# Kernel optimization log

Hardware: AMD Instinct MI355X
Metric: run time of the kernel (lower is better)

Reference implementation:

```python
import jax, jax.numpy as jnp
import numpy as np

D = 4096      # input_size == hidden_size (required by the broadcast add in the update)
T = 8192      # sequence length
F = 10        # num_factor (hard-coded in the module)
OUT = 10      # output_size
BETA = 0.1    # exponential scale for decay factors


def setup_inputs() -> dict:
    key = jax.random.key(0)
    ks = jax.random.split(key, 4)
    inp = jax.random.normal(ks[0], (T, 1, D), dtype=jnp.float32)
    hidden = jnp.zeros((1, F, D), dtype=jnp.float32)
    # decay factors: 1 - clip(Exp(beta), 0, 1-eps), each broadcast across hidden dim
    rng = np.random.default_rng(0)
    d = 1.0 - np.clip(rng.exponential(BETA, F), 0.0, 1.0 - np.finfo(np.float32).eps)
    w = jnp.broadcast_to(jnp.asarray(d, jnp.float32)[None, :, None], (1, F, D))
    pool_w = jax.random.normal(ks[1], (1, F, 1), jnp.float32) * (1.0 / np.sqrt(F))
    pool_b = jnp.zeros((1,), jnp.float32)
    H1 = (D + D) // 2  # (input_size + hidden_size) // 2
    i2o_w = jax.random.normal(ks[2], (H1, 2 * D), jnp.float32) * (1.0 / np.sqrt(2 * D))
    i2o_b = jnp.zeros((H1,), jnp.float32)
    o_w = jax.random.normal(ks[3], (OUT, H1), jnp.float32) * (1.0 / np.sqrt(H1))
    o_b = jnp.zeros((OUT,), jnp.float32)
    return dict(inp=inp, hidden=hidden, w=w, pool_w=pool_w, pool_b=pool_b,
                i2o_w=i2o_w, i2o_b=i2o_b, o_w=o_w, o_b=o_b)


def reference(inp, hidden, w, pool_w, pool_b, i2o_w, i2o_b, o_w, o_b):
    # inp: [T, 1, D]; hidden: [1, F, D] decay-state
    Tn = inp.shape[0]

    def step(carry, xt):
        h, hsum = carry
        hsum = hsum + h                   # pre-update hidden feeds the pooled feature
        h_new = w * h + xt[:, None, :]    # decay-weighted update, x broadcast over factors
        return (h_new, hsum), None

    (h_final, h_sum), _ = jax.lax.scan(step, (hidden, jnp.zeros_like(hidden)), inp)

    # Conv1d(F, 1, 1) pooling is linear -> sum over time of pool(h_t) = pool(sum_t h_t)
    pooled_sum = jnp.einsum('f,bfd->bd', pool_w[0, :, 0], h_sum) + Tn * pool_b  # [1, D]
    x_sum = inp.sum(axis=0)  # [1, D]

    # avg_feature at the last step = cumulative sum of combined / steps
    avg = jnp.concatenate([x_sum, pooled_sum], axis=1) / Tn  # [1, 2D]
    pred = jax.nn.relu(avg @ i2o_w.T + i2o_b) @ o_w.T + o_b  # [1, OUT]
    return pred, h_final
```

## Files before the change

kernel.cpp:

```cpp
#include <hip/hip_runtime.h>

#define TLEN 8192
#define DD   4096
#define NF   10
#define NC   12
#define NACC 12

__device__ __forceinline__ double powi_d(double w, int n) {
    double a = 1.0, p = w;
    while (n) { if (n & 1) a *= p; p *= p; n >>= 1; }
    return a;
}

__global__ void coef_kernel(const float* __restrict__ w,
                            const float* __restrict__ pool_w,
                            float* __restrict__ coef) {
    int t = blockIdx.x * blockDim.x + threadIdx.x;
    if (t >= TLEN) return;
    int n = TLEN - 1 - t;
    double g = 0.0;
#pragma unroll
    for (int f = 0; f < NF; ++f) {
        double wf = (double)w[(size_t)f * DD];
        double a  = powi_d(wf, n);
        double den = 1.0 - wf;
        double c  = (den > 1e-30) ? (1.0 - a) / den : (double)n;
        g += (double)pool_w[f] * c;
        coef[t * NC + f] = (float)a;
    }
    coef[t * NC + NF]     = (float)g;
    coef[t * NC + NF + 1] = 0.0f;
}

__global__ __launch_bounds__(256) void pass_kernel(const float* __restrict__ inp,
                                                   const float* __restrict__ coef,
                                                   float* __restrict__ part,
                                                   int rows) {
    __shared__ float sc[256 * NC];
    const int t0 = blockIdx.y * rows;
    const int d  = blockIdx.x * 1024 + threadIdx.x * 4;

    float sx=0,sy=0,sz=0,sw=0;
    float px=0,py=0,pz=0,pw4=0;
    float hx[NF], hy[NF], hz[NF], hw[NF];
#pragma unroll
    for (int f = 0; f < NF; ++f) { hx[f]=0; hy[f]=0; hz[f]=0; hw[f]=0; }

    const float* ip = inp + (size_t)t0 * DD + d;

    for (int rbase = 0; rbase < rows; rbase += 256) {
        int rcnt = rows - rbase; if (rcnt > 256) rcnt = 256;
        __syncthreads();
        for (int i = threadIdx.x; i < rcnt * NC; i += 256)
            sc[i] = coef[(size_t)(t0 + rbase) * NC + i];
        __syncthreads();
        for (int r = 0; r < rcnt; ++r) {
            float4 x = *(const float4*)ip;
            ip += DD;
            const float* cf = &sc[r * NC];
            sx += x.x; sy += x.y; sz += x.z; sw += x.w;
            float g = cf[NF];
            px  = fmaf(g, x.x, px);  py  = fmaf(g, x.y, py);
            pz  = fmaf(g, x.z, pz);  pw4 = fmaf(g, x.w, pw4);
#pragma unroll
            for (int f = 0; f < NF; ++f) {
                float a = cf[f];
                hx[f] = fmaf(a, x.x, hx[f]); hy[f] = fmaf(a, x.y, hy[f]);
                hz[f] = fmaf(a, x.z, hz[f]); hw[f] = fmaf(a, x.w, hw[f]);
            }
        }
    }

    size_t base = ((size_t)blockIdx.y * NC) * DD + d;
    *(float4*)(part + base)      = make_float4(sx, sy, sz, sw);
    *(float4*)(part + base + DD) = make_float4(px, py, pz, pw4);
#pragma unroll
    for (int f = 0; f < NF; ++f)
        *(float4*)(part + base + (size_t)(2 + f) * DD) =
            make_float4(hx[f], hy[f], hz[f], hw[f]);
}

__global__ void reduce_kernel(const float* __restrict__ part,
                              float* __restrict__ red, int C) {
    int idx = blockIdx.x * blockDim.x + threadIdx.x;
    if (idx >= NACC * DD) return;
    float s = 0.0f;
    for (int c = 0; c < C; ++c)
        s += part[(size_t)c * NC * DD + idx];
    red[idx] = s;
}

__global__ void finalize_kernel(const float* __restrict__ red,
                                const float* __restrict__ w,
                                const float* __restrict__ pool_w,
                                const float* __restrict__ pool_b,
                                const float* __restrict__ hidden,
                                float* __restrict__ out,
                                float* __restrict__ avg) {
    int i = blockIdx.x * blockDim.x + threadIdx.x;
    int d = i * 4;
    float4 xs = *(const float4*)(red + d);
    float4 pl = *(const float4*)(red + DD + d);
    const float invT = 1.0f / (float)TLEN;
#pragma unroll
    for (int f = 0; f < NF; ++f) {
        double wf = (double)w[(size_t)f * DD];
        double wTd = powi_d(wf, TLEN);
        double den = 1.0 - wf;
        double sTd = (den > 1e-30) ? (1.0 - wTd) / den : (double)TLEN;
        float wT = (float)wTd;
        float pwsT = (float)((double)pool_w[f] * sTd);
        float4 hf = *(const float4*)(red + (size_t)(2 + f) * DD + d);
        float4 h0 = *(const float4*)(hidden + (size_t)f * DD + d);
        hf.x = fmaf(wT, h0.x, hf.x); hf.y = fmaf(wT, h0.y, hf.y);
        hf.z = fmaf(wT, h0.z, hf.z); hf.w = fmaf(wT, h0.w, hf.w);
        pl.x = fmaf(pwsT, h0.x, pl.x); pl.y = fmaf(pwsT, h0.y, pl.y);
        pl.z = fmaf(pwsT, h0.z, pl.z); pl.w = fmaf(pwsT, h0.w, pl.w);
        float* o = out + 10 + (size_t)f * DD + d;
        o[0] = hf.x; o[1] = hf.y; o[2] = hf.z; o[3] = hf.w;
    }
    float pb = pool_b[0];
    avg[d+0] = xs.x * invT; avg[d+1] = xs.y * invT;
    avg[d+2] = xs.z * invT; avg[d+3] = xs.w * invT;
    avg[DD + d + 0] = pl.x * invT + pb; avg[DD + d + 1] = pl.y * invT + pb;
    avg[DD + d + 2] = pl.z * invT + pb; avg[DD + d + 3] = pl.w * invT + pb;
}

__global__ __launch_bounds__(256) void gemv_kernel(const float* __restrict__ W,
                                                   const float* __restrict__ b,
                                                   const float* __restrict__ avg,
                                                   float* __restrict__ hid) {
    int row  = blockIdx.x * 4 + (threadIdx.x >> 6);
    int lane = threadIdx.x & 63;
    const float* wr = W + (size_t)row * (2 * DD);
    float acc = 0.0f;
#pragma unroll 8
    for (int j0 = 0; j0 < 32; ++j0) {
        int j = j0 * 256 + lane * 4;
        float4 wv = *(const float4*)(wr + j);
        float4 av = *(const float4*)(avg + j);
        acc = fmaf(wv.x, av.x, acc); acc = fmaf(wv.y, av.y, acc);
        acc = fmaf(wv.z, av.z, acc); acc = fmaf(wv.w, av.w, acc);
    }
    for (int off = 32; off; off >>= 1) acc += __shfl_down(acc, off, 64);
    if (lane == 0) hid[row] = fmaxf(acc + b[row], 0.0f);
}

__global__ void out_kernel(const float* __restrict__ hid,
                           const float* __restrict__ ow,
                           const float* __restrict__ ob,
                           float* __restrict__ out) {
    __shared__ float redl[256];
    int o = blockIdx.x;
    float acc = 0.0f;
    for (int h = threadIdx.x; h < DD; h += 256)
        acc = fmaf(hid[h], ow[(size_t)o * DD + h], acc);
    redl[threadIdx.x] = acc;
    __syncthreads();
    for (int s = 128; s; s >>= 1) {
        if (threadIdx.x < s) redl[threadIdx.x] += redl[threadIdx.x + s];
        __syncthreads();
    }
    if (threadIdx.x == 0) out[o] = redl[0] + ob[o];
}

extern "C" void kernel_launch(void* const* d_in, const int* in_sizes, int n_in,
                              void* d_out, int out_size, void* d_ws, size_t ws_size,
                              hipStream_t stream) {
    const float* inp    = (const float*)d_in[0];
    const float* hidden = (const float*)d_in[1];
    const float* w      = (const float*)d_in[2];
    const float* pw     = (const float*)d_in[3];
    const float* pb     = (const float*)d_in[4];
    const float* i2o_w  = (const float*)d_in[5];
    const float* i2o_b  = (const float*)d_in[6];
    const float* o_w    = (const float*)d_in[7];
    const float* o_b    = (const float*)d_in[8];
    float* out = (float*)d_out;
    float* ws  = (float*)d_ws;

    float* coef = ws;
    float* red  = ws + 98304;
    float* avg  = ws + 147456;
    float* hid  = ws + 155648;
    float* part = ws + 159744;

    int C = 128;
    while (C > 1) {
        size_t need = (159744 + (size_t)C * NC * DD) * sizeof(float);
        if (need <= ws_size) break;
        C >>= 1;
    }
    int rows = TLEN / C;

    coef_kernel<<<TLEN / 256, 256, 0, stream>>>(w, pw, coef);
    pass_kernel<<<dim3(4, C), 256, 0, stream>>>(inp, coef, part, rows);
    reduce_kernel<<<(NACC * DD + 255) / 256, 256, 0, stream>>>(part, red, C);
    finalize_kernel<<<4, 256, 0, stream>>>(red, w, pw, pb, hidden, out, avg);
    gemv_kernel<<<DD / 4, 256, 0, stream>>>(i2o_w, i2o_b, avg, hid);
    out_kernel<<<10, 256, 0, stream>>>(hid, o_w, o_b, out);
}
```

Baseline: 113.4 us.

## Fuse coefficient computation into pass kernel, prefetch rows, stage avg in LDS

```diff
diff --git a/kernel.cpp b/kernel.cpp
--- a/kernel.cpp
+++ b/kernel.cpp
@@ -12,33 +12,35 @@
     return a;
 }
 
-__global__ void coef_kernel(const float* __restrict__ w,
-                            const float* __restrict__ pool_w,
-                            float* __restrict__ coef) {
-    int t = blockIdx.x * blockDim.x + threadIdx.x;
-    if (t >= TLEN) return;
-    int n = TLEN - 1 - t;
-    double g = 0.0;
-#pragma unroll
-    for (int f = 0; f < NF; ++f) {
-        double wf = (double)w[(size_t)f * DD];
-        double a  = powi_d(wf, n);
-        double den = 1.0 - wf;
-        double c  = (den > 1e-30) ? (1.0 - a) / den : (double)n;
-        g += (double)pool_w[f] * c;
-        coef[t * NC + f] = (float)a;
-    }
-    coef[t * NC + NF]     = (float)g;
-    coef[t * NC + NF + 1] = 0.0f;
-}
-
 __global__ __launch_bounds__(256) void pass_kernel(const float* __restrict__ inp,
-                                                   const float* __restrict__ coef,
+                                                   const float* __restrict__ w,
+                                                   const float* __restrict__ pool_w,
                                                    float* __restrict__ part,
                                                    int rows) {
     __shared__ float sc[256 * NC];
+    __shared__ float scg[256 * NF];
     const int t0 = blockIdx.y * rows;
-    const int d  = blockIdx.x * 1024 + threadIdx.x * 4;
+
+    for (int i = threadIdx.x; i < rows * NF; i += 256) {
+        int r = i / NF, f = i - r * NF;
+        double wf = (double)w[(size_t)f * DD];
+        int n = TLEN - 1 - (t0 + r);
+        double a = powi_d(wf, n);
+        double den = 1.0 - wf;
+        sc[r * NC + f] = (float)a;
+        scg[i] = (float)((den > 1e-12) ? (double)pool_w[f] * (1.0 - a) / den
+                                       : (double)pool_w[f] * (double)n);
+    }
+    __syncthreads();
+    if (threadIdx.x < rows) {
+        float g = 0.0f;
+#pragma unroll
+        for (int f = 0; f < NF; ++f) g += scg[threadIdx.x * NF + f];
+        sc[threadIdx.x * NC + NF] = g;
+    }
+    __syncthreads();
+
+    const int d = blockIdx.x * 1024 + threadIdx.x * 4;
 
     float sx=0,sy=0,sz=0,sw=0;
     float px=0,py=0,pz=0,pw4=0;
@@ -46,30 +48,37 @@
 #pragma unroll
     for (int f = 0; f < NF; ++f) { hx[f]=0; hy[f]=0; hz[f]=0; hw[f]=0; }
 
+    auto PROC = [&](int r, float4 x) {
+        const float* cf = &sc[r * NC];
+        sx += x.x; sy += x.y; sz += x.z; sw += x.w;
+        float g = cf[NF];
+        px  = fmaf(g, x.x, px);  py  = fmaf(g, x.y, py);
+        pz  = fmaf(g, x.z, pz);  pw4 = fmaf(g, x.w, pw4);
+#pragma unroll
+        for (int f = 0; f < NF; ++f) {
+            float a = cf[f];
+            hx[f] = fmaf(a, x.x, hx[f]); hy[f] = fmaf(a, x.y, hy[f]);
+            hz[f] = fmaf(a, x.z, hz[f]); hw[f] = fmaf(a, x.w, hw[f]);
+        }
+    };
+
     const float* ip = inp + (size_t)t0 * DD + d;
-
-    for (int rbase = 0; rbase < rows; rbase += 256) {
-        int rcnt = rows - rbase; if (rcnt > 256) rcnt = 256;
-        __syncthreads();
-        for (int i = threadIdx.x; i < rcnt * NC; i += 256)
-            sc[i] = coef[(size_t)(t0 + rbase) * NC + i];
-        __syncthreads();
-        for (int r = 0; r < rcnt; ++r) {
-            float4 x = *(const float4*)ip;
-            ip += DD;
-            const float* cf = &sc[r * NC];
-            sx += x.x; sy += x.y; sz += x.z; sw += x.w;
-            float g = cf[NF];
-            px  = fmaf(g, x.x, px);  py  = fmaf(g, x.y, py);
-            pz  = fmaf(g, x.z, pz);  pw4 = fmaf(g, x.w, pw4);
-#pragma unroll
-            for (int f = 0; f < NF; ++f) {
-                float a = cf[f];
-                hx[f] = fmaf(a, x.x, hx[f]); hy[f] = fmaf(a, x.y, hy[f]);
-                hz[f] = fmaf(a, x.z, hz[f]); hw[f] = fmaf(a, x.w, hw[f]);
-            }
-        }
-    }
+    float4 xa = *(const float4*)(ip);
+    float4 xb = *(const float4*)(ip + DD);
+    float4 xc = *(const float4*)(ip + 2 * DD);
+    float4 xd = *(const float4*)(ip + 3 * DD);
+    ip += 4 * (size_t)DD;
+    int r = 0;
+    for (; r + 4 < rows; r += 4) {
+        float4 ya = *(const float4*)(ip);
+        float4 yb = *(const float4*)(ip + DD);
+        float4 yc = *(const float4*)(ip + 2 * DD);
+        float4 yd = *(const float4*)(ip + 3 * DD);
+        ip += 4 * (size_t)DD;
+        PROC(r + 0, xa); PROC(r + 1, xb); PROC(r + 2, xc); PROC(r + 3, xd);
+        xa = ya; xb = yb; xc = yc; xd = yd;
+    }
+    PROC(r + 0, xa); PROC(r + 1, xb); PROC(r + 2, xc); PROC(r + 3, xd);
 
     size_t base = ((size_t)blockIdx.y * NC) * DD + d;
     *(float4*)(part + base)      = make_float4(sx, sy, sz, sw);
@@ -107,7 +116,7 @@
         double wf = (double)w[(size_t)f * DD];
         double wTd = powi_d(wf, TLEN);
         double den = 1.0 - wf;
-        double sTd = (den > 1e-30) ? (1.0 - wTd) / den : (double)TLEN;
+        double sTd = (den > 1e-12) ? (1.0 - wTd) / den : (double)TLEN;
         float wT = (float)wTd;
         float pwsT = (float)((double)pool_w[f] * sTd);
         float4 hf = *(const float4*)(red + (size_t)(2 + f) * DD + d);
@@ -130,18 +139,27 @@
                                                    const float* __restrict__ b,
                                                    const float* __restrict__ avg,
                                                    float* __restrict__ hid) {
+    __shared__ float sa[2 * DD];
+    for (int i = threadIdx.x * 4; i < 2 * DD; i += 1024)
+        *(float4*)(sa + i) = *(const float4*)(avg + i);
+    __syncthreads();
     int row  = blockIdx.x * 4 + (threadIdx.x >> 6);
     int lane = threadIdx.x & 63;
-    const float* wr = W + (size_t)row * (2 * DD);
-    float acc = 0.0f;
+    const float* wr = W + (size_t)row * (2 * DD) + lane * 4;
+    const float* ar = sa + lane * 4;
+    float acc0 = 0.0f, acc1 = 0.0f;
 #pragma unroll 8
-    for (int j0 = 0; j0 < 32; ++j0) {
-        int j = j0 * 256 + lane * 4;
-        float4 wv = *(const float4*)(wr + j);
-        float4 av = *(const float4*)(avg + j);
-        acc = fmaf(wv.x, av.x, acc); acc = fmaf(wv.y, av.y, acc);
-        acc = fmaf(wv.z, av.z, acc); acc = fmaf(wv.w, av.w, acc);
-    }
+    for (int g = 0; g < 32; g += 2) {
+        float4 w0 = *(const float4*)(wr + g * 256);
+        float4 w1 = *(const float4*)(wr + g * 256 + 256);
+        float4 a0 = *(const float4*)(ar + g * 256);
+        float4 a1 = *(const float4*)(ar + g * 256 + 256);
+        acc0 = fmaf(w0.x, a0.x, acc0); acc0 = fmaf(w0.y, a0.y, acc0);
+        acc0 = fmaf(w0.z, a0.z, acc0); acc0 = fmaf(w0.w, a0.w, acc0);
+        acc1 = fmaf(w1.x, a1.x, acc1); acc1 = fmaf(w1.y, a1.y, acc1);
+        acc1 = fmaf(w1.z, a1.z, acc1); acc1 = fmaf(w1.w, a1.w, acc1);
+    }
+    float acc = acc0 + acc1;
     for (int off = 32; off; off >>= 1) acc += __shfl_down(acc, off, 64);
     if (lane == 0) hid[row] = fmaxf(acc + b[row], 0.0f);
 }
@@ -179,22 +197,20 @@
     float* out = (float*)d_out;
     float* ws  = (float*)d_ws;
 
-    float* coef = ws;
-    float* red  = ws + 98304;
-    float* avg  = ws + 147456;
-    float* hid  = ws + 155648;
-    float* part = ws + 159744;
-
-    int C = 128;
-    while (C > 1) {
-        size_t need = (159744 + (size_t)C * NC * DD) * sizeof(float);
+    float* red  = ws;
+    float* avg  = ws + 49152;
+    float* hid  = ws + 57344;
+    float* part = ws + 61440;
+
+    int C = 256;
+    while (C > 32) {
+        size_t need = (61440 + (size_t)C * NC * DD) * sizeof(float);
         if (need <= ws_size) break;
         C >>= 1;
     }
     int rows = TLEN / C;
 
-    coef_kernel<<<TLEN / 256, 256, 0, stream>>>(w, pw, coef);
-    pass_kernel<<<dim3(4, C), 256, 0, stream>>>(inp, coef, part, rows);
+    pass_kernel<<<dim3(4, C), 256, 0, stream>>>(inp, w, pw, part, rows);
     reduce_kernel<<<(NACC * DD + 255) / 256, 256, 0, stream>>>(part, red, C);
     finalize_kernel<<<4, 256, 0, stream>>>(red, w, pw, pb, hidden, out, avg);
     gemv_kernel<<<DD / 4, 256, 0, stream>>>(i2o_w, i2o_b, avg, hid);
```

Result: slower. 139.8 us (+23.3%).

## Split partial reduction into two stages and pad partial stride

Applied to the files above, without the earlier changes.

```diff
diff --git a/kernel.cpp b/kernel.cpp
--- a/kernel.cpp
+++ b/kernel.cpp
@@ -5,6 +5,8 @@
 #define NF   10
 #define NC   12
 #define NACC 12
+#define CCH  128
+#define PSTRIDE (NC * DD + 256)
 
 __device__ __forceinline__ double powi_d(double w, int n) {
     double a = 1.0, p = w;
@@ -71,7 +73,7 @@
         }
     }
 
-    size_t base = ((size_t)blockIdx.y * NC) * DD + d;
+    size_t base = (size_t)blockIdx.y * PSTRIDE + d;
     *(float4*)(part + base)      = make_float4(sx, sy, sz, sw);
     *(float4*)(part + base + DD) = make_float4(px, py, pz, pw4);
 #pragma unroll
@@ -80,17 +82,18 @@
             make_float4(hx[f], hy[f], hz[f], hw[f]);
 }
 
-__global__ void reduce_kernel(const float* __restrict__ part,
-                              float* __restrict__ red, int C) {
-    int idx = blockIdx.x * blockDim.x + threadIdx.x;
-    if (idx >= NACC * DD) return;
+__global__ __launch_bounds__(256) void reduce1_kernel(const float* __restrict__ part,
+                                                      float* __restrict__ p2) {
+    int idx = blockIdx.x * 256 + threadIdx.x;
+    int c0  = blockIdx.y * 8;
     float s = 0.0f;
-    for (int c = 0; c < C; ++c)
-        s += part[(size_t)c * NC * DD + idx];
-    red[idx] = s;
-}
-
-__global__ void finalize_kernel(const float* __restrict__ red,
+#pragma unroll
+    for (int k = 0; k < 8; ++k)
+        s += part[(size_t)(c0 + k) * PSTRIDE + idx];
+    p2[(size_t)blockIdx.y * (NACC * DD) + idx] = s;
+}
+
+__global__ void finalize_kernel(const float* __restrict__ p2,
                                 const float* __restrict__ w,
                                 const float* __restrict__ pool_w,
                                 const float* __restrict__ pool_b,
@@ -99,8 +102,20 @@
                                 float* __restrict__ avg) {
     int i = blockIdx.x * blockDim.x + threadIdx.x;
     int d = i * 4;
-    float4 xs = *(const float4*)(red + d);
-    float4 pl = *(const float4*)(red + DD + d);
+
+    auto SUM16 = [&](int acc) -> float4 {
+        float4 s = make_float4(0.f, 0.f, 0.f, 0.f);
+#pragma unroll
+        for (int g = 0; g < 16; ++g) {
+            float4 v = *(const float4*)(p2 + (size_t)g * (NACC * DD)
+                                           + (size_t)acc * DD + d);
+            s.x += v.x; s.y += v.y; s.z += v.z; s.w += v.w;
+        }
+        return s;
+    };
+
+    float4 xs = SUM16(0);
+    float4 pl = SUM16(1);
     const float invT = 1.0f / (float)TLEN;
 #pragma unroll
     for (int f = 0; f < NF; ++f) {
@@ -110,7 +125,7 @@
         double sTd = (den > 1e-30) ? (1.0 - wTd) / den : (double)TLEN;
         float wT = (float)wTd;
         float pwsT = (float)((double)pool_w[f] * sTd);
-        float4 hf = *(const float4*)(red + (size_t)(2 + f) * DD + d);
+        float4 hf = SUM16(2 + f);
         float4 h0 = *(const float4*)(hidden + (size_t)f * DD + d);
         hf.x = fmaf(wT, h0.x, hf.x); hf.y = fmaf(wT, h0.y, hf.y);
         hf.z = fmaf(wT, h0.z, hf.z); hf.w = fmaf(wT, h0.w, hf.w);
@@ -180,23 +195,17 @@
     float* ws  = (float*)d_ws;
 
     float* coef = ws;
-    float* red  = ws + 98304;
-    float* avg  = ws + 147456;
-    float* hid  = ws + 155648;
-    float* part = ws + 159744;
-
-    int C = 128;
-    while (C > 1) {
-        size_t need = (159744 + (size_t)C * NC * DD) * sizeof(float);
-        if (need <= ws_size) break;
-        C >>= 1;
-    }
-    int rows = TLEN / C;
+    float* p2   = ws + 98304;
+    float* avg  = ws + 884736;
+    float* hid  = ws + 892928;
+    float* part = ws + 897024;
+
+    const int rows = TLEN / CCH;
 
     coef_kernel<<<TLEN / 256, 256, 0, stream>>>(w, pw, coef);
-    pass_kernel<<<dim3(4, C), 256, 0, stream>>>(inp, coef, part, rows);
-    reduce_kernel<<<(NACC * DD + 255) / 256, 256, 0, stream>>>(part, red, C);
-    finalize_kernel<<<4, 256, 0, stream>>>(red, w, pw, pb, hidden, out, avg);
+    pass_kernel<<<dim3(4, CCH), 256, 0, stream>>>(inp, coef, part, rows);
+    reduce1_kernel<<<dim3(192, 16), 256, 0, stream>>>(part, p2);
+    finalize_kernel<<<4, 256, 0, stream>>>(p2, w, pw, pb, hidden, out, avg);
     gemv_kernel<<<DD / 4, 256, 0, stream>>>(i2o_w, i2o_b, avg, hid);
     out_kernel<<<10, 256, 0, stream>>>(hid, o_w, o_b, out);
 }
```

After: 124.5 us. +9.8%, slower.

## Fuse all stages into one cooperative kernel with grid-wide syncs

Applied to the files above, without the earlier changes.

```diff
diff --git a/kernel.cpp b/kernel.cpp
--- a/kernel.cpp
+++ b/kernel.cpp
@@ -1,15 +1,186 @@
 #include <hip/hip_runtime.h>
+#include <hip/hip_cooperative_groups.h>
+
+namespace cg = cooperative_groups;
 
 #define TLEN 8192
 #define DD   4096
 #define NF   10
 #define NC   12
 #define NACC 12
+#define CCH  128
+#define ROWS 64
 
 __device__ __forceinline__ double powi_d(double w, int n) {
     double a = 1.0, p = w;
     while (n) { if (n & 1) a *= p; p *= p; n >>= 1; }
     return a;
+}
+
+__global__ __launch_bounds__(256) void fused_kernel(
+    const float* __restrict__ inp,   const float* __restrict__ hidden,
+    const float* __restrict__ w,     const float* __restrict__ pool_w,
+    const float* __restrict__ pool_b,
+    const float* __restrict__ W1,    const float* __restrict__ b1,
+    const float* __restrict__ W2,    const float* __restrict__ b2,
+    float* __restrict__ out,
+    float* __restrict__ part, float* __restrict__ red,
+    float* __restrict__ avg,  float* __restrict__ hid)
+{
+    cg::grid_group grid = cg::this_grid();
+    const int tid = threadIdx.x;
+    const int bid = blockIdx.x;
+
+    __shared__ float sc [ROWS * NC];
+    __shared__ float scg[ROWS * NF];
+    __shared__ float redl[256];
+
+    {
+        const int cgp = bid & 3;
+        const int ch  = bid >> 2;
+        const int t0  = ch * ROWS;
+
+        for (int i = tid; i < ROWS * NF; i += 256) {
+            int r = i / NF, f = i - r * NF;
+            double wf = (double)w[(size_t)f * DD];
+            int n = TLEN - 1 - (t0 + r);
+            double a = powi_d(wf, n);
+            double den = 1.0 - wf;
+            sc[r * NC + f] = (float)a;
+            scg[i] = (float)((den > 1e-30) ? (double)pool_w[f] * (1.0 - a) / den
+                                           : (double)pool_w[f] * (double)n);
+        }
+        __syncthreads();
+        if (tid < ROWS) {
+            float g = 0.0f;
+#pragma unroll
+            for (int f = 0; f < NF; ++f) g += scg[tid * NF + f];
+            sc[tid * NC + NF] = g;
+        }
+        __syncthreads();
+
+        const int d = cgp * 1024 + tid * 4;
+        float sx=0,sy=0,sz=0,sw=0;
+        float px=0,py=0,pz=0,pw4=0;
+        float hx[NF], hy[NF], hz[NF], hw[NF];
+#pragma unroll
+        for (int f = 0; f < NF; ++f) { hx[f]=0; hy[f]=0; hz[f]=0; hw[f]=0; }
+
+        const float* ip = inp + (size_t)t0 * DD + d;
+        for (int r = 0; r < ROWS; ++r) {
+            float4 x = *(const float4*)ip;
+            ip += DD;
+            const float* cf = &sc[r * NC];
+            sx += x.x; sy += x.y; sz += x.z; sw += x.w;
+            float g = cf[NF];
+            px  = fmaf(g, x.x, px);  py  = fmaf(g, x.y, py);
+            pz  = fmaf(g, x.z, pz);  pw4 = fmaf(g, x.w, pw4);
+#pragma unroll
+            for (int f = 0; f < NF; ++f) {
+                float a = cf[f];
+                hx[f] = fmaf(a, x.x, hx[f]); hy[f] = fmaf(a, x.y, hy[f]);
+                hz[f] = fmaf(a, x.z, hz[f]); hw[f] = fmaf(a, x.w, hw[f]);
+            }
+        }
+
+        size_t base = ((size_t)ch * NACC) * DD + d;
+        *(float4*)(part + base)      = make_float4(sx, sy, sz, sw);
+        *(float4*)(part + base + DD) = make_float4(px, py, pz, pw4);
+#pragma unroll
+        for (int f = 0; f < NF; ++f)
+            *(float4*)(part + base + (size_t)(2 + f) * DD) =
+                make_float4(hx[f], hy[f], hz[f], hw[f]);
+    }
+    grid.sync();
+
+    {
+        int idx = bid * 256 + tid;
+        if (idx < NACC * DD) {
+            float s0=0,s1=0,s2=0,s3=0,s4=0,s5=0,s6=0,s7=0;
+            for (int c = 0; c < CCH; c += 8) {
+                s0 += part[(size_t)(c+0) * (NACC*DD) + idx];
+                s1 += part[(size_t)(c+1) * (NACC*DD) + idx];
+                s2 += part[(size_t)(c+2) * (NACC*DD) + idx];
+                s3 += part[(size_t)(c+3) * (NACC*DD) + idx];
+                s4 += part[(size_t)(c+4) * (NACC*DD) + idx];
+                s5 += part[(size_t)(c+5) * (NACC*DD) + idx];
+                s6 += part[(size_t)(c+6) * (NACC*DD) + idx];
+                s7 += part[(size_t)(c+7) * (NACC*DD) + idx];
+            }
+            red[idx] = ((s0+s1)+(s2+s3)) + ((s4+s5)+(s6+s7));
+        }
+    }
+    grid.sync();
+
+    {
+        if (bid < 4) {
+            int i = bid * 256 + tid;
+            int d = i * 4;
+            float4 xs = *(const float4*)(red + d);
+            float4 pl = *(const float4*)(red + DD + d);
+            const float invT = 1.0f / (float)TLEN;
+#pragma unroll
+            for (int f = 0; f < NF; ++f) {
+                double wf = (double)w[(size_t)f * DD];
+                double wTd = powi_d(wf, TLEN);
+                double den = 1.0 - wf;
+                double sTd = (den > 1e-30) ? (1.0 - wTd) / den : (double)TLEN;
+                float wT = (float)wTd;
+                float pwsT = (float)((double)pool_w[f] * sTd);
+                float4 hf = *(const float4*)(red + (size_t)(2 + f) * DD + d);
+                float4 h0 = *(const float4*)(hidden + (size_t)f * DD + d);
+                hf.x = fmaf(wT, h0.x, hf.x); hf.y = fmaf(wT, h0.y, hf.y);
+                hf.z = fmaf(wT, h0.z, hf.z); hf.w = fmaf(wT, h0.w, hf.w);
+                pl.x = fmaf(pwsT, h0.x, pl.x); pl.y = fmaf(pwsT, h0.y, pl.y);
+                pl.z = fmaf(pwsT, h0.z, pl.z); pl.w = fmaf(pwsT, h0.w, pl.w);
+                float* o = out + 10 + (size_t)f * DD + d;
+                o[0] = hf.x; o[1] = hf.y; o[2] = hf.z; o[3] = hf.w;
+            }
+            float pb = pool_b[0];
+            avg[d+0] = xs.x * invT; avg[d+1] = xs.y * invT;
+            avg[d+2] = xs.z * invT; avg[d+3] = xs.w * invT;
+            avg[DD + d + 0] = pl.x * invT + pb; avg[DD + d + 1] = pl.y * invT + pb;
+            avg[DD + d + 2] = pl.z * invT + pb; avg[DD + d + 3] = pl.w * invT + pb;
+        }
+    }
+    grid.sync();
+
+    {
+        int wave = tid >> 6, lane = tid & 63;
+#pragma unroll
+        for (int rr = 0; rr < 2; ++rr) {
+            int row = bid * 8 + wave * 2 + rr;
+            const float* wr = W1 + (size_t)row * (2 * DD);
+            float acc = 0.0f;
+#pragma unroll 8
+            for (int j0 = 0; j0 < 32; ++j0) {
+                int j = j0 * 256 + lane * 4;
+                float4 wv = *(const float4*)(wr + j);
+                float4 av = *(const float4*)(avg + j);
+                acc = fmaf(wv.x, av.x, acc); acc = fmaf(wv.y, av.y, acc);
+                acc = fmaf(wv.z, av.z, acc); acc = fmaf(wv.w, av.w, acc);
+            }
+            for (int off = 32; off; off >>= 1) acc += __shfl_down(acc, off, 64);
+            if (lane == 0) hid[row] = fmaxf(acc + b1[row], 0.0f);
+        }
+    }
+    grid.sync();
+
+    {
+        if (bid < 10) {
+            int o = bid;
+            float acc = 0.0f;
+            for (int h = tid; h < DD; h += 256)
+                acc = fmaf(hid[h], W2[(size_t)o * DD + h], acc);
+            redl[tid] = acc;
+            __syncthreads();
+            for (int s = 128; s; s >>= 1) {
+                if (tid < s) redl[tid] += redl[tid + s];
+                __syncthreads();
+            }
+            if (tid == 0) out[o] = redl[0] + b2[o];
+        }
+    }
 }
 
 __global__ void coef_kernel(const float* __restrict__ w,
@@ -39,15 +210,11 @@
     __shared__ float sc[256 * NC];
     const int t0 = blockIdx.y * rows;
     const int d  = blockIdx.x * 1024 + threadIdx.x * 4;
-
-    float sx=0,sy=0,sz=0,sw=0;
-    float px=0,py=0,pz=0,pw4=0;
+    float sx=0,sy=0,sz=0,sw=0, px=0,py=0,pz=0,pw4=0;
     float hx[NF], hy[NF], hz[NF], hw[NF];
 #pragma unroll
     for (int f = 0; f < NF; ++f) { hx[f]=0; hy[f]=0; hz[f]=0; hw[f]=0; }
-
     const float* ip = inp + (size_t)t0 * DD + d;
-
     for (int rbase = 0; rbase < rows; rbase += 256) {
         int rcnt = rows - rbase; if (rcnt > 256) rcnt = 256;
         __syncthreads();
@@ -55,8 +222,7 @@
             sc[i] = coef[(size_t)(t0 + rbase) * NC + i];
         __syncthreads();
         for (int r = 0; r < rcnt; ++r) {
-            float4 x = *(const float4*)ip;
-            ip += DD;
+            float4 x = *(const float4*)ip; ip += DD;
             const float* cf = &sc[r * NC];
             sx += x.x; sy += x.y; sz += x.z; sw += x.w;
             float g = cf[NF];
@@ -70,8 +236,7 @@
             }
         }
     }
-
-    size_t base = ((size_t)blockIdx.y * NC) * DD + d;
+    size_t base = ((size_t)blockIdx.y * NACC) * DD + d;
     *(float4*)(part + base)      = make_float4(sx, sy, sz, sw);
     *(float4*)(part + base + DD) = make_float4(px, py, pz, pw4);
 #pragma unroll
@@ -86,7 +251,7 @@
     if (idx >= NACC * DD) return;
     float s = 0.0f;
     for (int c = 0; c < C; ++c)
-        s += part[(size_t)c * NC * DD + idx];
+        s += part[(size_t)c * (NACC*DD) + idx];
     red[idx] = s;
 }
 
@@ -185,18 +350,21 @@
     float* hid  = ws + 155648;
     float* part = ws + 159744;
 
-    int C = 128;
-    while (C > 1) {
-        size_t need = (159744 + (size_t)C * NC * DD) * sizeof(float);
-        if (need <= ws_size) break;
-        C >>= 1;
-    }
-    int rows = TLEN / C;
-
-    coef_kernel<<<TLEN / 256, 256, 0, stream>>>(w, pw, coef);
-    pass_kernel<<<dim3(4, C), 256, 0, stream>>>(inp, coef, part, rows);
-    reduce_kernel<<<(NACC * DD + 255) / 256, 256, 0, stream>>>(part, red, C);
-    finalize_kernel<<<4, 256, 0, stream>>>(red, w, pw, pb, hidden, out, avg);
-    gemv_kernel<<<DD / 4, 256, 0, stream>>>(i2o_w, i2o_b, avg, hid);
-    out_kernel<<<10, 256, 0, stream>>>(hid, o_w, o_b, out);
-}
+    void* args[] = {
+        (void*)&inp, (void*)&hidden, (void*)&w, (void*)&pw, (void*)&pb,
+        (void*)&i2o_w, (void*)&i2o_b, (void*)&o_w, (void*)&o_b,
+        (void*)&out, (void*)&part, (void*)&red, (void*)&avg, (void*)&hid
+    };
+    hipError_t err = hipLaunchCooperativeKernel((const void*)fused_kernel,
+                                                dim3(512), dim3(256),
+                                                args, 0, stream);
+    if (err != hipSuccess) {
+        const int C = CCH, rows = TLEN / CCH;
+        coef_kernel<<<TLEN / 256, 256, 0, stream>>>(w, pw, coef);
+        pass_kernel<<<dim3(4, C), 256, 0, stream>>>(inp, coef, part, rows);
+        reduce_kernel<<<(NACC * DD + 255) / 256, 256, 0, stream>>>(part, red, C);
+        finalize_kernel<<<4, 256, 0, stream>>>(red, w, pw, pb, hidden, out, avg);
+        gemv_kernel<<<DD / 4, 256, 0, stream>>>(i2o_w, i2o_b, avg, hid);
+        out_kernel<<<10, 256, 0, stream>>>(hid, o_w, o_b, out);
+    }
+}
```

New measurement: 321.2 us. +183.2%, slower.
